# Kernel optimization log

Measured on AMD Instinct MI355X. Metric: run time of the kernel, lower is better.

## Reference

```python
import jax, jax.numpy as jnp
import numpy as np

# EXP-HYDRO concrete realization of HydrologyModel.
# Parameter order matches _parameter_bounds key order; bounds per standard EXP-HYDRO.
PARAM_BOUNDS = [
    ("f",    0.0,  0.1),
    ("Smax", 100.0, 1500.0),
    ("Qmax", 10.0, 50.0),
    ("Df",   0.0,  5.0),
    ("Tmax", 0.0,  3.0),
    ("Tmin", -3.0, 0.0),
]
NEARZERO = 1e-6
T_STEPS = 1024
N_BASINS = 8192
N_PARAMS = len(PARAM_BOUNDS)


def _denormalize(static_params_norm):
    # sigmoid activation then affine map to bounds; returns dict name -> [B]
    act = jax.nn.sigmoid(static_params_norm)  # [B, P]
    return {name: lo + (hi - lo) * act[:, i]
            for i, (name, lo, hi) in enumerate(PARAM_BOUNDS)}


def _run_core(prcp, temp, pet, params, nearzero=NEARZERO):
    # prcp/temp/pet: [T, B]; params: dict of [B]
    f, Smax, Qmax = params["f"], params["Smax"], params["Qmax"]
    Df, Tmax, Tmin = params["Df"], params["Tmax"], params["Tmin"]

    def step(states, forc_t):
        snowpack, soilwater = states
        prcp_t, temp_t, pet_t = forc_t
        # hydroflux formulas (elementwise over basins)
        snowfall = jnp.where(temp_t < Tmin, prcp_t, 0.0)
        rainfall = prcp_t - snowfall
        melt = jnp.minimum(snowpack, Df * jnp.maximum(temp_t - Tmax, 0.0))
        evap = pet_t * jnp.minimum(soilwater / Smax, 1.0)
        baseflow = Qmax * jnp.exp(-f * jnp.maximum(Smax - soilwater, 0.0))
        surfaceflow = jnp.maximum(soilwater - Smax, 0.0)
        # stateflux formulas (state changes)
        d_snow = snowfall - melt
        d_soil = rainfall + melt - evap - baseflow - surfaceflow
        # state update with clamp(min=nearzero)
        new_snow = jnp.maximum(snowpack + d_snow, nearzero)
        new_soil = jnp.maximum(soilwater + d_soil, nearzero)
        out = jnp.stack([snowfall, rainfall, melt, evap,
                         baseflow, surfaceflow, d_snow, d_soil])  # [8, B]
        return (new_snow, new_soil), out

    B = prcp.shape[1]
    init = (jnp.zeros((B,), prcp.dtype), jnp.zeros((B,), prcp.dtype))
    _, outs = jax.lax.scan(step, init, (prcp, temp, pet))
    return outs  # [T, 8, B]


def setup_inputs() -> dict:
    key = jax.random.key(0)
    k1, k2, k3, k4 = jax.random.split(key, 4)
    prcp = jax.random.uniform(k1, (T_STEPS, N_BASINS), jnp.float32) * 10.0  # mm/day
    temp = jax.random.normal(k2, (T_STEPS, N_BASINS), jnp.float32) * 5.0    # deg C
    pet = jax.random.uniform(k3, (T_STEPS, N_BASINS), jnp.float32) * 5.0    # mm/day
    static_params_norm = jax.random.normal(k4, (N_BASINS, N_PARAMS), jnp.float32)
    return {"prcp": prcp, "temp": temp, "pet": pet,
            "static_params_norm": static_params_norm}


def reference(prcp, temp, pet, static_params_norm):
    params = _denormalize(static_params_norm)
    return _run_core(prcp, temp, pet, params)  # [T, 8, B]
```

## Files before the change

### kernel.cpp

```cpp
#include <hip/hip_runtime.h>
#include <stdint.h>

#define NB 8192
#define OUT_TSTRIDE (8 * NB)
#define TILE 32
#define LDS_F 6144

__device__ __forceinline__ float sigmoidf_(float x) {
    return 1.0f / (1.0f + __expf(-x));
}

__device__ __forceinline__ void async16(const float* g, float* l) {
    __builtin_amdgcn_global_load_lds(
        (const __attribute__((address_space(1))) void*)g,
        (__attribute__((address_space(3))) void*)l, 16, 0, 0);
}

__device__ __forceinline__ void fill_tile(const float* __restrict__ prcp,
                                          const float* __restrict__ temp,
                                          const float* __restrict__ pet,
                                          float* lds, int t0, int tid,
                                          int gbase) {
#pragma unroll
    for (int r = 0; r < 6; ++r) {
        const float* src = (r < 2) ? prcp : ((r < 4) ? temp : pet);
        int tt = ((r & 1) << 4) + (tid >> 4);
        int t  = t0 + tt;
        t      = (t > 1023) ? 1023 : t;
        const float* g = src + (size_t)t * NB + gbase + ((tid & 15) << 2);
        float* l       = lds + (r << 10) + (tid << 2);
        async16(g, l);
    }
}

template <int CP>
__device__ void run(const float* __restrict__ prcp,
                    const float* __restrict__ temp,
                    const float* __restrict__ pet, float* __restrict__ out,
                    float (*lds)[LDS_F], int tid, int lane, int gbase,
                    int basin, int ntiles, int lo1, int hi1, int lo2, int hi2,
                    float f, float Smax, float Qmax, float Df, float Tmax,
                    float Tmin) {
    const float rSmax = 1.0f / Smax;
    const float nf    = -f;
    float snow = 0.0f, soil = 0.0f;
    float* const outBase = out + (size_t)(2 * CP) * NB + basin;

    fill_tile(prcp, temp, pet, lds[0], 0, tid, gbase);
    __syncthreads();

    for (int tile = 0; tile < ntiles; ++tile) {
        const int cur = tile & 1;
        fill_tile(prcp, temp, pet, lds[cur ^ 1], (tile + 1) * TILE, tid, gbase);

        const bool doStore =
            (tile >= lo1 && tile < hi1) || (tile >= lo2 && tile < hi2);
        const float* lp = lds[cur];
        float* o        = outBase + (size_t)tile * TILE * OUT_TSTRIDE;
#pragma unroll
        for (int i = 0; i < TILE; ++i) {
            const float P  = lp[i * 64 + lane];
            const float Tm = lp[2048 + i * 64 + lane];
            const float Pe = lp[4096 + i * 64 + lane];

            const float snowfall    = (Tm < Tmin) ? P : 0.0f;
            const float rainfall    = P - snowfall;
            const float melt        = fminf(snow, Df * fmaxf(Tm - Tmax, 0.0f));
            const float evap        = Pe * fminf(soil * rSmax, 1.0f);
            const float baseflow    = Qmax * __expf(nf * fmaxf(Smax - soil, 0.0f));
            const float surfaceflow = fmaxf(soil - Smax, 0.0f);
            const float d_snow      = snowfall - melt;
            const float d_soil =
                (((rainfall + melt) - evap) - baseflow) - surfaceflow;
            snow = fmaxf(snow + d_snow, 1e-6f);
            soil = fmaxf(soil + d_soil, 1e-6f);

            if (doStore) {
                float sv0, sv1;
                if (CP == 0)      { sv0 = snowfall; sv1 = rainfall; }
                else if (CP == 1) { sv0 = melt;     sv1 = evap; }
                else if (CP == 2) { sv0 = baseflow; sv1 = surfaceflow; }
                else              { sv0 = d_snow;   sv1 = d_soil; }
                o[(size_t)i * OUT_TSTRIDE]      = sv0;
                o[(size_t)i * OUT_TSTRIDE + NB] = sv1;
            }
        }
        __syncthreads();
    }
}

extern "C" __global__ void __launch_bounds__(256, 2)
    hydro_kernel(const float* __restrict__ prcp, const float* __restrict__ temp,
                 const float* __restrict__ pet, const float* __restrict__ spn,
                 float* __restrict__ out) {
    __shared__ float lds[2][LDS_F];

    const int tid  = threadIdx.x;
    const int lane = tid & 63;
    const int w    = tid >> 6;
    const int b    = blockIdx.x;
    const int idx  = b & 255;
    const int pass = b >> 8;
    const int group = (idx >> 4) * 8 + (idx & 7);
    const int t01   = (idx >> 3) & 1;
    const int type  = pass ? (3 - t01) : t01;
    const int gbase = group * 64;
    const int basin = gbase + lane;

    const int ntiles = (8 - type) * 4;
    const int lo1    = type * 4;
    const int hi1    = lo1 + 4;
    const int lo2    = (7 - type) * 4;
    const int hi2    = lo2 + 4;

    const float* p6  = spn + basin * 6;
    const float f    = 0.1f * sigmoidf_(p6[0]);
    const float Smax = 100.0f + 1400.0f * sigmoidf_(p6[1]);
    const float Qmax = 10.0f + 40.0f * sigmoidf_(p6[2]);
    const float Df   = 5.0f * sigmoidf_(p6[3]);
    const float Tmax = 3.0f * sigmoidf_(p6[4]);
    const float Tmin = -3.0f + 3.0f * sigmoidf_(p6[5]);

    switch (__builtin_amdgcn_readfirstlane(w)) {
        case 0:
            run<0>(prcp, temp, pet, out, lds, tid, lane, gbase, basin, ntiles,
                   lo1, hi1, lo2, hi2, f, Smax, Qmax, Df, Tmax, Tmin);
            break;
        case 1:
            run<1>(prcp, temp, pet, out, lds, tid, lane, gbase, basin, ntiles,
                   lo1, hi1, lo2, hi2, f, Smax, Qmax, Df, Tmax, Tmin);
            break;
        case 2:
            run<2>(prcp, temp, pet, out, lds, tid, lane, gbase, basin, ntiles,
                   lo1, hi1, lo2, hi2, f, Smax, Qmax, Df, Tmax, Tmin);
            break;
        default:
            run<3>(prcp, temp, pet, out, lds, tid, lane, gbase, basin, ntiles,
                   lo1, hi1, lo2, hi2, f, Smax, Qmax, Df, Tmax, Tmin);
            break;
    }
}

extern "C" void kernel_launch(void* const* d_in, const int* in_sizes, int n_in,
                              void* d_out, int out_size, void* d_ws,
                              size_t ws_size, hipStream_t stream) {
    const float* prcp = (const float*)d_in[0];
    const float* temp = (const float*)d_in[1];
    const float* pet  = (const float*)d_in[2];
    const float* spn  = (const float*)d_in[3];
    float* out        = (float*)d_out;

    hydro_kernel<<<dim3(512), dim3(256), 0, stream>>>(prcp, temp, pet, spn, out);
}
```

Baseline: 367.8 us.

## Split scan into checkpoint pass and parallel segment replay with full output writes

Replaces the single kernel, which replayed the recurrence redundantly per output pair, with two kernels. A lightweight first kernel runs the recurrence once per basin group and saves snow/soil state every SEGLEN steps into workspace. A second kernel launches one wave per (group, segment), restarts from the checkpoint and writes all eight fluxes directly. The intent is to expose far more parallelism for the output-write phase, at the cost of a serial 128-wave phase-1 pass with low occupancy and a second launch. Outputs must match exactly because the replay repeats the same arithmetic from the saved states.

```diff
diff --git a/kernel.cpp b/kernel.cpp
--- a/kernel.cpp
+++ b/kernel.cpp
@@ -2,9 +2,11 @@
 #include <stdint.h>
 
 #define NB 8192
+#define TSTEPS 1024
 #define OUT_TSTRIDE (8 * NB)
 #define TILE 32
 #define LDS_F 6144
+
 
 __device__ __forceinline__ float sigmoidf_(float x) {
     return 1.0f / (1.0f + __expf(-x));
@@ -16,128 +18,145 @@
         (__attribute__((address_space(3))) void*)l, 16, 0, 0);
 }
 
-__device__ __forceinline__ void fill_tile(const float* __restrict__ prcp,
-                                          const float* __restrict__ temp,
-                                          const float* __restrict__ pet,
-                                          float* lds, int t0, int tid,
-                                          int gbase) {
+struct Params {
+    float f, Smax, Qmax, Df, Tmax, Tmin, rSmax, nf;
+};
+
+__device__ __forceinline__ Params load_params(const float* __restrict__ spn,
+                                              int basin) {
+    const float* p6 = spn + (size_t)basin * 6;
+    Params p;
+    p.f     = 0.1f * sigmoidf_(p6[0]);
+    p.Smax  = 100.0f + 1400.0f * sigmoidf_(p6[1]);
+    p.Qmax  = 10.0f + 40.0f * sigmoidf_(p6[2]);
+    p.Df    = 5.0f * sigmoidf_(p6[3]);
+    p.Tmax  = 3.0f * sigmoidf_(p6[4]);
+    p.Tmin  = -3.0f + 3.0f * sigmoidf_(p6[5]);
+    p.rSmax = 1.0f / p.Smax;
+    p.nf    = -p.f;
+    return p;
+}
+
+struct Flux {
+    float snowfall, rainfall, melt, evap, baseflow, surfaceflow, d_snow, d_soil;
+};
+
+__device__ __forceinline__ Flux hydro_step(const Params& p, float& snow,
+                                           float& soil, float P, float Tm,
+                                           float Pe) {
+    Flux o;
+    o.snowfall    = (Tm < p.Tmin) ? P : 0.0f;
+    o.rainfall    = P - o.snowfall;
+    o.melt        = fminf(snow, p.Df * fmaxf(Tm - p.Tmax, 0.0f));
+    o.evap        = Pe * fminf(soil * p.rSmax, 1.0f);
+    o.baseflow    = p.Qmax * __expf(p.nf * fmaxf(p.Smax - soil, 0.0f));
+    o.surfaceflow = fmaxf(soil - p.Smax, 0.0f);
+    o.d_snow      = o.snowfall - o.melt;
+    o.d_soil = (((o.rainfall + o.melt) - o.evap) - o.baseflow) - o.surfaceflow;
+    snow = fmaxf(snow + o.d_snow, 1e-6f);
+    soil = fmaxf(soil + o.d_soil, 1e-6f);
+    return o;
+}
+
+__device__ __forceinline__ void fill64(const float* __restrict__ prcp,
+                                       const float* __restrict__ temp,
+                                       const float* __restrict__ pet,
+                                       float* lds, int t0, int lane,
+                                       int gbase) {
 #pragma unroll
-    for (int r = 0; r < 6; ++r) {
-        const float* src = (r < 2) ? prcp : ((r < 4) ? temp : pet);
-        int tt = ((r & 1) << 4) + (tid >> 4);
-        int t  = t0 + tt;
-        t      = (t > 1023) ? 1023 : t;
-        const float* g = src + (size_t)t * NB + gbase + ((tid & 15) << 2);
-        float* l       = lds + (r << 10) + (tid << 2);
+    for (int k = 0; k < 24; ++k) {
+        const float* src = (k < 8) ? prcp : ((k < 16) ? temp : pet);
+        int row = ((k & 7) << 2) + (lane >> 4);
+        int t   = t0 + row;
+        t       = (t > TSTEPS - 1) ? (TSTEPS - 1) : t;
+        const float* g = src + (size_t)t * NB + gbase + ((lane & 15) << 2);
+        float* l       = lds + (k << 8) + (lane << 2);
         async16(g, l);
     }
 }
 
-template <int CP>
-__device__ void run(const float* __restrict__ prcp,
-                    const float* __restrict__ temp,
-                    const float* __restrict__ pet, float* __restrict__ out,
-                    float (*lds)[LDS_F], int tid, int lane, int gbase,
-                    int basin, int ntiles, int lo1, int hi1, int lo2, int hi2,
-                    float f, float Smax, float Qmax, float Df, float Tmax,
-                    float Tmin) {
-    const float rSmax = 1.0f / Smax;
-    const float nf    = -f;
+template <int SEGLEN>
+__global__ void __launch_bounds__(64)
+hydro_phase1(const float* __restrict__ prcp, const float* __restrict__ temp,
+             const float* __restrict__ pet, const float* __restrict__ spn,
+             float* __restrict__ ckpt) {
+    __shared__ float lds[2][LDS_F];
+    const int lane  = threadIdx.x;
+    const int g     = blockIdx.x;
+    const int gbase = g * 64;
+    const int basin = gbase + lane;
+
+    const Params prm = load_params(spn, basin);
     float snow = 0.0f, soil = 0.0f;
-    float* const outBase = out + (size_t)(2 * CP) * NB + basin;
 
-    fill_tile(prcp, temp, pet, lds[0], 0, tid, gbase);
+    fill64(prcp, temp, pet, lds[0], 0, lane, gbase);
     __syncthreads();
 
-    for (int tile = 0; tile < ntiles; ++tile) {
+    for (int tile = 0; tile < TSTEPS / TILE; ++tile) {
         const int cur = tile & 1;
-        fill_tile(prcp, temp, pet, lds[cur ^ 1], (tile + 1) * TILE, tid, gbase);
+        fill64(prcp, temp, pet, lds[cur ^ 1], (tile + 1) * TILE, lane, gbase);
 
-        const bool doStore =
-            (tile >= lo1 && tile < hi1) || (tile >= lo2 && tile < hi2);
         const float* lp = lds[cur];
-        float* o        = outBase + (size_t)tile * TILE * OUT_TSTRIDE;
-#pragma unroll
+#pragma unroll 16
         for (int i = 0; i < TILE; ++i) {
+            const int t = tile * TILE + i;
+            if ((t & (SEGLEN - 1)) == 0) {
+                const int s = t / SEGLEN;
+                ckpt[(size_t)(2 * s) * NB + basin]     = snow;
+                ckpt[(size_t)(2 * s + 1) * NB + basin] = soil;
+            }
             const float P  = lp[i * 64 + lane];
             const float Tm = lp[2048 + i * 64 + lane];
             const float Pe = lp[4096 + i * 64 + lane];
-
-            const float snowfall    = (Tm < Tmin) ? P : 0.0f;
-            const float rainfall    = P - snowfall;
-            const float melt        = fminf(snow, Df * fmaxf(Tm - Tmax, 0.0f));
-            const float evap        = Pe * fminf(soil * rSmax, 1.0f);
-            const float baseflow    = Qmax * __expf(nf * fmaxf(Smax - soil, 0.0f));
-            const float surfaceflow = fmaxf(soil - Smax, 0.0f);
-            const float d_snow      = snowfall - melt;
-            const float d_soil =
-                (((rainfall + melt) - evap) - baseflow) - surfaceflow;
-            snow = fmaxf(snow + d_snow, 1e-6f);
-            soil = fmaxf(soil + d_soil, 1e-6f);
-
-            if (doStore) {
-                float sv0, sv1;
-                if (CP == 0)      { sv0 = snowfall; sv1 = rainfall; }
-                else if (CP == 1) { sv0 = melt;     sv1 = evap; }
-                else if (CP == 2) { sv0 = baseflow; sv1 = surfaceflow; }
-                else              { sv0 = d_snow;   sv1 = d_soil; }
-                o[(size_t)i * OUT_TSTRIDE]      = sv0;
-                o[(size_t)i * OUT_TSTRIDE + NB] = sv1;
-            }
+            (void)hydro_step(prm, snow, soil, P, Tm, Pe);
         }
         __syncthreads();
     }
 }
 
-extern "C" __global__ void __launch_bounds__(256, 2)
-    hydro_kernel(const float* __restrict__ prcp, const float* __restrict__ temp,
-                 const float* __restrict__ pet, const float* __restrict__ spn,
-                 float* __restrict__ out) {
-    __shared__ float lds[2][LDS_F];
+template <int SEGLEN>
+__global__ void __launch_bounds__(256, 4)
+hydro_phase2(const float* __restrict__ prcp, const float* __restrict__ temp,
+             const float* __restrict__ pet, const float* __restrict__ spn,
+             const float* __restrict__ ckpt, float* __restrict__ out) {
+    const int tid   = threadIdx.x;
+    const int lane  = tid & 63;
+    const int wid   = (blockIdx.x << 2) + (tid >> 6);
+    const int g     = wid & 127;
+    const int s     = wid >> 7;
+    const int basin = g * 64 + lane;
 
-    const int tid  = threadIdx.x;
-    const int lane = tid & 63;
-    const int w    = tid >> 6;
-    const int b    = blockIdx.x;
-    const int idx  = b & 255;
-    const int pass = b >> 8;
-    const int group = (idx >> 4) * 8 + (idx & 7);
-    const int t01   = (idx >> 3) & 1;
-    const int type  = pass ? (3 - t01) : t01;
-    const int gbase = group * 64;
-    const int basin = gbase + lane;
+    const Params prm = load_params(spn, basin);
 
-    const int ntiles = (8 - type) * 4;
-    const int lo1    = type * 4;
-    const int hi1    = lo1 + 4;
-    const int lo2    = (7 - type) * 4;
-    const int hi2    = lo2 + 4;
+    float snow, soil;
+    if (SEGLEN == 1024) {
+        snow = 0.0f;
+        soil = 0.0f;
+    } else {
+        snow = ckpt[(size_t)(2 * s) * NB + basin];
+        soil = ckpt[(size_t)(2 * s + 1) * NB + basin];
+    }
 
-    const float* p6  = spn + basin * 6;
-    const float f    = 0.1f * sigmoidf_(p6[0]);
-    const float Smax = 100.0f + 1400.0f * sigmoidf_(p6[1]);
-    const float Qmax = 10.0f + 40.0f * sigmoidf_(p6[2]);
-    const float Df   = 5.0f * sigmoidf_(p6[3]);
-    const float Tmax = 3.0f * sigmoidf_(p6[4]);
-    const float Tmin = -3.0f + 3.0f * sigmoidf_(p6[5]);
+    const int t0 = s * SEGLEN;
+#pragma unroll 8
+    for (int i = 0; i < SEGLEN; ++i) {
+        const int t     = t0 + i;
+        const size_t fo = (size_t)t * NB + basin;
+        const float P   = prcp[fo];
+        const float Tm  = temp[fo];
+        const float Pe  = pet[fo];
 
-    switch (__builtin_amdgcn_readfirstlane(w)) {
-        case 0:
-            run<0>(prcp, temp, pet, out, lds, tid, lane, gbase, basin, ntiles,
-                   lo1, hi1, lo2, hi2, f, Smax, Qmax, Df, Tmax, Tmin);
-            break;
-        case 1:
-            run<1>(prcp, temp, pet, out, lds, tid, lane, gbase, basin, ntiles,
-                   lo1, hi1, lo2, hi2, f, Smax, Qmax, Df, Tmax, Tmin);
-            break;
-        case 2:
-            run<2>(prcp, temp, pet, out, lds, tid, lane, gbase, basin, ntiles,
-                   lo1, hi1, lo2, hi2, f, Smax, Qmax, Df, Tmax, Tmin);
-            break;
-        default:
-            run<3>(prcp, temp, pet, out, lds, tid, lane, gbase, basin, ntiles,
-                   lo1, hi1, lo2, hi2, f, Smax, Qmax, Df, Tmax, Tmin);
-            break;
+        const Flux fl = hydro_step(prm, snow, soil, P, Tm, Pe);
+
+        float* o = out + (size_t)t * OUT_TSTRIDE + basin;
+        o[0 * NB] = fl.snowfall;
+        o[1 * NB] = fl.rainfall;
+        o[2 * NB] = fl.melt;
+        o[3 * NB] = fl.evap;
+        o[4 * NB] = fl.baseflow;
+        o[5 * NB] = fl.surfaceflow;
+        o[6 * NB] = fl.d_snow;
+        o[7 * NB] = fl.d_soil;
     }
 }
 
@@ -149,6 +168,23 @@
     const float* pet  = (const float*)d_in[2];
     const float* spn  = (const float*)d_in[3];
     float* out        = (float*)d_out;
+    float* ckpt       = (float*)d_ws;
 
-    hydro_kernel<<<dim3(512), dim3(256), 0, stream>>>(prcp, temp, pet, spn, out);
+    const size_t need32  = (size_t)(TSTEPS / 32) * 2 * NB * sizeof(float);
+    const size_t need128 = (size_t)(TSTEPS / 128) * 2 * NB * sizeof(float);
+
+    if (ws_size >= need32) {
+        hydro_phase1<32><<<dim3(128), dim3(64), 0, stream>>>(prcp, temp, pet,
+                                                             spn, ckpt);
+        hydro_phase2<32><<<dim3(1024), dim3(256), 0, stream>>>(
+            prcp, temp, pet, spn, ckpt, out);
+    } else if (ws_size >= need128) {
+        hydro_phase1<128><<<dim3(128), dim3(64), 0, stream>>>(prcp, temp, pet,
+                                                              spn, ckpt);
+        hydro_phase2<128><<<dim3(256), dim3(256), 0, stream>>>(
+            prcp, temp, pet, spn, ckpt, out);
+    } else {
+        hydro_phase2<1024><<<dim3(32), dim3(256), 0, stream>>>(
+            prcp, temp, pet, spn, nullptr, out);
+    }
 }
```

Result: slower. 400.2 us (+8.8%).
